# Kernel optimization log

Measured on AMD Instinct MI355X. Metric: run time of the kernel, lower is better.

## Reference

```python
import jax, jax.numpy as jnp
from jax import lax
import numpy as np

K = 3       # kernel_size
STRIDE = 1
PAD = 1
DIL = 1


def setup_inputs() -> dict:
    key = jax.random.key(0)
    k1, k2, k3, k4 = jax.random.split(key, 4)
    B, C, H, W, Co = 8, 128, 64, 64, 128
    x = jax.random.normal(k1, (B, C, H, W), jnp.float32)
    # offset conv: deformable_groups * 2 * K * K = 18 output channels
    w_off = jax.random.normal(k2, (2 * K * K, C, K, K), jnp.float32) * 0.01
    b_off = jax.random.normal(k3, (2 * K * K,), jnp.float32) * 0.01
    w_dcn = jax.random.normal(k4, (Co, C, K, K), jnp.float32) * (1.0 / np.sqrt(C * K * K))
    return {"x": x, "w_off": w_off, "b_off": b_off, "w_dcn": w_dcn}


def _deform_conv(x, w_off, b_off, w_dcn):
    B, C, H, W = x.shape
    Ho = (H + 2 * PAD - DIL * (K - 1) - 1) // STRIDE + 1
    Wo = (W + 2 * PAD - DIL * (K - 1) - 1) // STRIDE + 1
    KK = K * K

    # --- offset branch: standard conv2d ---
    offset = lax.conv_general_dilated(
        x, w_off, window_strides=(STRIDE, STRIDE),
        padding=[(PAD, PAD), (PAD, PAD)], rhs_dilation=(DIL, DIL),
        dimension_numbers=("NCHW", "OIHW", "NCHW"))
    offset = offset + b_off[None, :, None, None]          # [B, 2*KK, Ho, Wo]
    off = offset.reshape(B, KK, 2, Ho, Wo)
    dy, dx = off[:, :, 0], off[:, :, 1]                   # [B, KK, Ho, Wo]

    # --- sampling coordinates: p0 + p_k + offset ---
    ky, kx = jnp.meshgrid(jnp.arange(K), jnp.arange(K), indexing="ij")
    ky = (ky.reshape(-1) * DIL).astype(x.dtype)           # [KK]
    kx = (kx.reshape(-1) * DIL).astype(x.dtype)
    base_y = (jnp.arange(Ho) * STRIDE - PAD).astype(x.dtype)[None, :, None] + ky[:, None, None]
    base_x = (jnp.arange(Wo) * STRIDE - PAD).astype(x.dtype)[None, None, :] + kx[:, None, None]
    y = base_y[None] + dy                                 # [B, KK, Ho, Wo]
    xc = base_x[None] + dx

    y0 = jnp.floor(y)
    x0 = jnp.floor(xc)
    wy = y - y0                                           # bilinear weights
    wx = xc - x0
    y0i = y0.astype(jnp.int32)
    x0i = x0.astype(jnp.int32)

    def sample_one(xb, y0i, x0i, wy, wx):
        # xb: [C, H, W]; index tensors: [KK, Ho, Wo]
        xf = xb.reshape(C, H * W)

        def corner(iy, ix):
            valid = (iy >= 0) & (iy < H) & (ix >= 0) & (ix < W)   # zero padding
            idx = jnp.clip(iy, 0, H - 1) * W + jnp.clip(ix, 0, W - 1)
            v = jnp.take(xf, idx.reshape(-1), axis=1).reshape(C, KK, Ho, Wo)
            return v * valid[None].astype(xb.dtype)

        v00 = corner(y0i, x0i)
        v01 = corner(y0i, x0i + 1)
        v10 = corner(y0i + 1, x0i)
        v11 = corner(y0i + 1, x0i + 1)
        return (v00 * (1 - wy) * (1 - wx) + v01 * (1 - wy) * wx
                + v10 * wy * (1 - wx) + v11 * wy * wx)      # [C, KK, Ho, Wo]

    sampled = jax.vmap(sample_one)(x, y0i, x0i, wy, wx)      # [B, C, KK, Ho, Wo]

    # --- deformable conv accumulation (groups=1, no bias) ---
    w = w_dcn.reshape(w_dcn.shape[0], C, KK)
    return jnp.einsum("bckhw,ock->bohw", sampled, w)


def reference(x, w_off, b_off, w_dcn):
    return _deform_conv(x, w_off, b_off, w_dcn)
```

## Files before the change

### kernel.cpp

```cpp
#include <hip/hip_runtime.h>

typedef float f32x4 __attribute__((ext_vector_type(4)));
typedef int   i32x4 __attribute__((ext_vector_type(4)));
typedef unsigned u32x4 __attribute__((ext_vector_type(4)));
typedef short b16x8 __attribute__((ext_vector_type(8)));

__device__ __forceinline__ short f2b(float v) {
  union { float f; unsigned u; } x; x.f = v;
  unsigned r = x.u + 0x7FFFu + ((x.u >> 16) & 1u);
  return (short)(r >> 16);
}
__device__ __forceinline__ float b2f(short s) {
  union { unsigned u; float f; } x; x.u = ((unsigned)(unsigned short)s) << 16;
  return x.f;
}

#define WT_ELEMS   (9 * 128 * 128)
#define WOFF_ELEMS (9 * 32 * 128)
#define XT_BYTES   (8u * 4096u * 128u * 2u)

#define WIN_OFF   0
#define SS0_OFF   23040
#define SS1_OFF   27136
#define COFS_OFF  31232
#define WTA_OFF   35840
#define ARENA_SZ  40448

__global__ __launch_bounds__(256) void prep_w(
    const float* __restrict__ w_off, const float* __restrict__ w_dcn,
    short* __restrict__ wT, short* __restrict__ wOffT)
{
  int t = blockIdx.x * 256 + threadIdx.x;
  int stride = gridDim.x * 256;
  for (int i = t; i < WT_ELEMS; i += stride) {
    int j    = i & 7;
    int lane = (i >> 3) & 63;
    int kk   = (i >> 9) & 3;
    int og   = (i >> 11) & 7;
    int k    = i >> 14;
    int o = og * 16 + (lane & 15);
    int c = kk * 32 + (lane >> 4) * 8 + j;
    wT[i] = f2b(w_dcn[o * 1152 + c * 9 + k]);
  }
  for (int i = t; i < WOFF_ELEMS; i += stride) {
    int j    = i & 7;
    int lane = (i >> 3) & 63;
    int kk   = (i >> 9) & 3;
    int fo   = (i >> 11) & 1;
    int k    = i >> 12;
    int o = fo * 16 + (lane & 15);
    int c = kk * 32 + (lane >> 4) * 8 + j;
    wOffT[i] = (o < 18) ? f2b(w_off[o * 1152 + c * 9 + k]) : (short)0;
  }
}

__global__ __launch_bounds__(256) void transp(
    const float* __restrict__ xg, short* __restrict__ xt)
{
  __shared__ float tile[32][65];
  const int bid = blockIdx.x;
  const int b = bid >> 6, y = bid & 63;
  const int t = threadIdx.x;
  const float* src = xg + ((size_t)b << 19) + y * 64;
  short*       dst = xt + ((size_t)b << 19) + (size_t)y * 8192;

  for (int ct = 0; ct < 4; ++ct) {
    __syncthreads();
    int c_l = t >> 3, w0 = (t & 7) * 8;
    const float* p = src + (size_t)(ct * 32 + c_l) * 4096 + w0;
    f32x4 a0 = *(const f32x4*)p;
    f32x4 a1 = *(const f32x4*)(p + 4);
    #pragma unroll
    for (int i = 0; i < 4; ++i) { tile[c_l][w0 + i] = a0[i]; tile[c_l][w0 + 4 + i] = a1[i]; }
    __syncthreads();
    int w = t >> 2, j0 = (t & 3) * 8;
    b16x8 pk;
    #pragma unroll
    for (int j = 0; j < 8; ++j) pk[j] = f2b(tile[j0 + j][w]);
    *(b16x8*)(dst + w * 128 + ct * 32 + j0) = pk;
  }
}

__device__ __forceinline__ void lerp_half(char* sbuf, const char* win, const short* xb,
                                          int h, const unsigned* cofsT, const f32x4* wtA,
                                          int k, int px_s, int cg) {
  u32x4 co = *(const u32x4*)&cofsT[(k * 32 + px_s) * 4];
  f32x4 wv = wtA[k * 32 + px_s];
  b16x8 g[4];
  #pragma unroll
  for (int c = 0; c < 4; ++c) {
    unsigned ofs = co[c];
    if (ofs & 0x80000000u) {
      const short* gp = xb + (size_t)(ofs & 0x7fffffffu) * 128 + h * 64 + cg * 8;
      g[c] = *(const b16x8*)gp;
    } else {
      unsigned key = ((ofs >> 7) & 7) << 4;
      g[c] = *(const b16x8*)(win + ofs + ((cg * 16) ^ key));
    }
  }
  b16x8 pk;
  #pragma unroll
  for (int j = 0; j < 8; ++j) {
    float v = wv[0] * b2f(g[0][j]) + wv[1] * b2f(g[1][j]) +
              wv[2] * b2f(g[2][j]) + wv[3] * b2f(g[3][j]);
    pk[j] = f2b(v);
  }
  *(b16x8*)(sbuf + px_s * 128 + ((cg * 16) ^ ((px_s & 7) << 4))) = pk;
}

__device__ __forceinline__ void load_wfrag_half(b16x8 (&w)[4], const short* wT,
                                                int k, int h, int wv_, int lane) {
  const int og0 = wv_ * 2;
  #pragma unroll
  for (int kkl = 0; kkl < 2; ++kkl) {
    w[kkl]     = *(const b16x8*)(wT + ((((k * 8 + og0)     * 4) + 2 * h + kkl) << 9) + lane * 8);
    w[2 + kkl] = *(const b16x8*)(wT + ((((k * 8 + og0 + 1) * 4) + 2 * h + kkl) << 9) + lane * 8);
  }
}

__device__ __forceinline__ void mfma_half(const char* sbuf, const b16x8 (&w)[4],
                                          int l15, int l4,
                                          f32x4& a00, f32x4& a01, f32x4& a10, f32x4& a11) {
  #pragma unroll
  for (int kkl = 0; kkl < 2; ++kkl) {
    int cl2 = kkl * 64 + l4 * 16;
    b16x8 b0 = *(const b16x8*)(sbuf + l15 * 128        + (cl2 ^ ((l15 & 7) << 4)));
    b16x8 b1 = *(const b16x8*)(sbuf + (16 + l15) * 128 + (cl2 ^ ((l15 & 7) << 4)));
    a00 = __builtin_amdgcn_mfma_f32_16x16x32_bf16(w[kkl],     b0, a00, 0, 0, 0);
    a01 = __builtin_amdgcn_mfma_f32_16x16x32_bf16(w[kkl],     b1, a01, 0, 0, 0);
    a10 = __builtin_amdgcn_mfma_f32_16x16x32_bf16(w[2 + kkl], b0, a10, 0, 0, 0);
    a11 = __builtin_amdgcn_mfma_f32_16x16x32_bf16(w[2 + kkl], b1, a11, 0, 0, 0);
  }
}

__global__ __launch_bounds__(256, 4) void dcn_mfma(
    const short* __restrict__ xt, const float* __restrict__ b_off,
    const short* __restrict__ wT, const short* __restrict__ wOffT,
    float* __restrict__ out)
{
  __shared__ __align__(16) char arena[ARENA_SZ];

  char*     sW    = arena + WIN_OFF;
  char*     win   = arena + WIN_OFF;
  char*     sS0   = arena + SS0_OFF;
  char*     sS1   = arena + SS1_OFF;
  float*    offT  = (float*)(arena + SS0_OFF);
  unsigned* cofsT = (unsigned*)(arena + COFS_OFF);
  f32x4*    wtA   = (f32x4*)(arena + WTA_OFF);

  const int tid  = threadIdx.x;
  const int lane = tid & 63;
  const int wv_  = tid >> 6;
  const int bid  = blockIdx.x;
  const int swz  = (bid & 7) * 128 + (bid >> 3);
  const int b    = swz >> 7;
  const int ho   = (swz >> 1) & 63;
  const int wo0  = (swz & 1) * 32;

  const int px_s = tid >> 3;
  const int cg   = tid & 7;
  const int l15  = lane & 15;
  const int l4   = lane >> 4;

  const short* xb = xt + ((size_t)b << 19);

  #pragma unroll 1
  for (int i = 0; i < 7; ++i) {
    int s = tid + i * 256;
    if (s < 1632) {
      int p = s >> 4, cc = s & 15;
      int py = p / 34, pxw = p - py * 34;
      int y = ho - 1 + py, xw = wo0 + pxw - 1;
      bool v = ((unsigned)y < 64u) && ((unsigned)xw < 64u);
      b16x8 q = {0,0,0,0,0,0,0,0};
      if (v) q = *(const b16x8*)(xb + ((size_t)(y * 64 + xw) << 7) + cc * 8);
      *(b16x8*)(sW + p * 256 + ((cc * 16) ^ ((p & 7) << 4))) = q;
    }
  }
  __syncthreads();

  f32x4 accP = {0.f, 0.f, 0.f, 0.f};
  const int fo = wv_ >> 1, fp = wv_ & 1;
  {
    const int bpx = fp * 16 + l15;
    #pragma unroll 1
    for (int k = 0; k < 9; ++k) {
      int ky = k / 3, kx = k - ky * 3;
      int p  = ky * 34 + bpx + kx;
      const short* wkf = wOffT + (((k * 2 + fo) * 4) << 9);
      #pragma unroll
      for (int kk = 0; kk < 4; ++kk) {
        int cf = kk * 32 + l4 * 8;
        b16x8 a  = *(const b16x8*)(wkf + (kk << 9) + lane * 8);
        b16x8 bb = *(const b16x8*)(sW + p * 256 + ((cf * 2) ^ ((p & 7) << 4)));
        accP = __builtin_amdgcn_mfma_f32_16x16x32_bf16(a, bb, accP, 0, 0, 0);
      }
    }
  }
  __syncthreads();
  {
    int px = fp * 16 + l15;
    int ob = fo * 16 + l4 * 4;
    #pragma unroll
    for (int r = 0; r < 4; ++r)
      offT[(ob + r) * 32 + px] = accP[r];
  }
  __syncthreads();

  #pragma unroll 1
  for (int i = 0; i < 2; ++i) {
    int item = tid + i * 256;
    if (item < 288) {
      int k = item >> 5, px = item & 31;
      int ky = k / 3, kx = k - ky * 3;
      float dy = offT[(2 * k) * 32 + px]     + b_off[2 * k];
      float dx = offT[(2 * k + 1) * 32 + px] + b_off[2 * k + 1];
      float yy = (float)(ho - 1 + ky) + dy;
      float xx = (float)(wo0 + px - 1 + kx) + dx;
      float y0f = floorf(yy), x0f = floorf(xx);
      float wy = yy - y0f, wx = xx - x0f;
      int y0 = (int)y0f, x0 = (int)x0f;
      int y1 = y0 + 1, x1 = x0 + 1;
      int cy0 = min(max(y0, 0), 63), cx0 = min(max(x0, 0), 63);
      int cy1 = min(max(y1, 0), 63), cx1 = min(max(x1, 0), 63);
      float vy0 = ((unsigned)y0 < 64u) ? 1.f : 0.f;
      float vy1 = ((unsigned)y1 < 64u) ? 1.f : 0.f;
      float vx0 = ((unsigned)x0 < 64u) ? 1.f : 0.f;
      float vx1 = ((unsigned)x1 < 64u) ? 1.f : 0.f;
      f32x4 wvv;
      wvv[0] = (1.f - wy) * (1.f - wx) * vy0 * vx0;
      wvv[1] = (1.f - wy) * wx         * vy0 * vx1;
      wvv[2] = wy         * (1.f - wx) * vy1 * vx0;
      wvv[3] = wy         * wx         * vy1 * vx1;
      int cys[4] = {cy0, cy0, cy1, cy1};
      int cxs[4] = {cx0, cx1, cx0, cx1};
      u32x4 enc;
      #pragma unroll
      for (int c = 0; c < 4; ++c) {
        int wr = cys[c] - (ho - 2);
        int wc = cxs[c] - (wo0 - 2);
        bool inw = ((unsigned)wr < 5u) && ((unsigned)wc < 36u);
        enc[c] = inw ? (unsigned)((wr * 36 + wc) * 128)
                     : (0x80000000u | (unsigned)(cys[c] * 64 + cxs[c]));
      }
      *(u32x4*)&cofsT[item * 4] = enc;
      wtA[item] = wvv;
    }
  }
  __syncthreads();

  f32x4 acc00 = {0,0,0,0}, acc01 = {0,0,0,0}, acc10 = {0,0,0,0}, acc11 = {0,0,0,0};
  b16x8 wreg[4], wnext[4];
  load_wfrag_half(wreg, wT, 0, 0, wv_, lane);

  #pragma unroll 1
  for (int h = 0; h < 2; ++h) {
    #pragma unroll 1
    for (int i = 0; i < 6; ++i) {
      int s = tid + i * 256;
      if (s < 1440) {
        int seg = s & 7, pos = s >> 3;
        int r = pos / 36, cc = pos - r * 36;
        int y = ho - 2 + r, x = wo0 - 2 + cc;
        bool v = ((unsigned)y < 64u) && ((unsigned)x < 64u);
        b16x8 q = {0,0,0,0,0,0,0,0};
        if (v) q = *(const b16x8*)(xb + ((size_t)(y * 64 + x) << 7) + h * 64 + seg * 8);
        *(b16x8*)(win + pos * 128 + ((seg * 16) ^ ((pos & 7) << 4))) = q;
      }
    }
    __syncthreads();

    #pragma unroll 1
    for (int k = 0; k < 9; ++k) {
      char* sb = ((h * 9 + k) & 1) ? sS1 : sS0;
      lerp_half(sb, win, xb, h, cofsT, wtA, k, px_s, cg);
      if (k < 8)            load_wfrag_half(wnext, wT, k + 1, h, wv_, lane);
      else if (h == 0)      load_wfrag_half(wnext, wT, 0, 1, wv_, lane);
      __syncthreads();
      mfma_half(sb, wreg, l15, l4, acc00, acc01, acc10, acc11);
      #pragma unroll
      for (int i = 0; i < 4; ++i) wreg[i] = wnext[i];
    }
  }

  {
    size_t base = ((size_t)b * 128) * 4096 + (size_t)ho * 64 + wo0;
    int o0 = wv_ * 32 + l4 * 4;
    #pragma unroll
    for (int r = 0; r < 4; ++r) {
      out[base + (size_t)(o0 + r) * 4096 + l15]           = acc00[r];
      out[base + (size_t)(o0 + r) * 4096 + 16 + l15]      = acc01[r];
      out[base + (size_t)(o0 + 16 + r) * 4096 + l15]      = acc10[r];
      out[base + (size_t)(o0 + 16 + r) * 4096 + 16 + l15] = acc11[r];
    }
  }
}

extern "C" void kernel_launch(void* const* d_in, const int* in_sizes, int n_in,
                              void* d_out, int out_size, void* d_ws, size_t ws_size,
                              hipStream_t stream) {
  const float* x     = (const float*)d_in[0];
  const float* w_off = (const float*)d_in[1];
  const float* b_off = (const float*)d_in[2];
  const float* w_dcn = (const float*)d_in[3];
  float* out = (float*)d_out;

  short* xt    = (short*)d_ws;
  short* wT    = (short*)((char*)d_ws + XT_BYTES);
  short* wOffT = (short*)((char*)d_ws + XT_BYTES + WT_ELEMS * 2);

  hipLaunchKernelGGL(prep_w,   dim3(64),   dim3(256), 0, stream, w_off, w_dcn, wT, wOffT);
  hipLaunchKernelGGL(transp,   dim3(512),  dim3(256), 0, stream, x, xt);
  hipLaunchKernelGGL(dcn_mfma, dim3(1024), dim3(256), 0, stream, xt, b_off, wT, wOffT, out);
}
```

Before: 52.08 us.

## Build MFMA B-fragments in registers directly from bilinear sampling

```diff
diff --git a/kernel.cpp b/kernel.cpp
--- a/kernel.cpp
+++ b/kernel.cpp
@@ -20,11 +20,10 @@
 #define XT_BYTES   (8u * 4096u * 128u * 2u)
 
 #define WIN_OFF   0
-#define SS0_OFF   23040
-#define SS1_OFF   27136
-#define COFS_OFF  31232
-#define WTA_OFF   35840
-#define ARENA_SZ  40448
+#define COFS_OFF  23040
+#define WTA_OFF   27648
+#define OFFT_OFF  32256
+#define ARENA_SZ  36352
 
 __global__ __launch_bounds__(256) void prep_w(
     const float* __restrict__ w_off, const float* __restrict__ w_dcn,
@@ -81,56 +80,28 @@
   }
 }
 
-__device__ __forceinline__ void lerp_half(char* sbuf, const char* win, const short* xb,
-                                          int h, const unsigned* cofsT, const f32x4* wtA,
-                                          int k, int px_s, int cg) {
-  u32x4 co = *(const u32x4*)&cofsT[(k * 32 + px_s) * 4];
-  f32x4 wv = wtA[k * 32 + px_s];
+__device__ __forceinline__ b16x8 lerp_frag(const char* win, const short* xb, int h,
+                                           u32x4 co, f32x4 wv, int ccol) {
   b16x8 g[4];
   #pragma unroll
   for (int c = 0; c < 4; ++c) {
     unsigned ofs = co[c];
     if (ofs & 0x80000000u) {
-      const short* gp = xb + (size_t)(ofs & 0x7fffffffu) * 128 + h * 64 + cg * 8;
+      const short* gp = xb + (size_t)(ofs & 0x7fffffffu) * 128 + h * 64 + (ccol >> 1);
       g[c] = *(const b16x8*)gp;
     } else {
       unsigned key = ((ofs >> 7) & 7) << 4;
-      g[c] = *(const b16x8*)(win + ofs + ((cg * 16) ^ key));
-    }
-  }
-  b16x8 pk;
+      g[c] = *(const b16x8*)(win + ofs + (ccol ^ key));
+    }
+  }
+  b16x8 sfrag;
   #pragma unroll
   for (int j = 0; j < 8; ++j) {
     float v = wv[0] * b2f(g[0][j]) + wv[1] * b2f(g[1][j]) +
               wv[2] * b2f(g[2][j]) + wv[3] * b2f(g[3][j]);
-    pk[j] = f2b(v);
-  }
-  *(b16x8*)(sbuf + px_s * 128 + ((cg * 16) ^ ((px_s & 7) << 4))) = pk;
-}
-
-__device__ __forceinline__ void load_wfrag_half(b16x8 (&w)[4], const short* wT,
-                                                int k, int h, int wv_, int lane) {
-  const int og0 = wv_ * 2;
-  #pragma unroll
-  for (int kkl = 0; kkl < 2; ++kkl) {
-    w[kkl]     = *(const b16x8*)(wT + ((((k * 8 + og0)     * 4) + 2 * h + kkl) << 9) + lane * 8);
-    w[2 + kkl] = *(const b16x8*)(wT + ((((k * 8 + og0 + 1) * 4) + 2 * h + kkl) << 9) + lane * 8);
-  }
-}
-
-__device__ __forceinline__ void mfma_half(const char* sbuf, const b16x8 (&w)[4],
-                                          int l15, int l4,
-                                          f32x4& a00, f32x4& a01, f32x4& a10, f32x4& a11) {
-  #pragma unroll
-  for (int kkl = 0; kkl < 2; ++kkl) {
-    int cl2 = kkl * 64 + l4 * 16;
-    b16x8 b0 = *(const b16x8*)(sbuf + l15 * 128        + (cl2 ^ ((l15 & 7) << 4)));
-    b16x8 b1 = *(const b16x8*)(sbuf + (16 + l15) * 128 + (cl2 ^ ((l15 & 7) << 4)));
-    a00 = __builtin_amdgcn_mfma_f32_16x16x32_bf16(w[kkl],     b0, a00, 0, 0, 0);
-    a01 = __builtin_amdgcn_mfma_f32_16x16x32_bf16(w[kkl],     b1, a01, 0, 0, 0);
-    a10 = __builtin_amdgcn_mfma_f32_16x16x32_bf16(w[2 + kkl], b0, a10, 0, 0, 0);
-    a11 = __builtin_amdgcn_mfma_f32_16x16x32_bf16(w[2 + kkl], b1, a11, 0, 0, 0);
-  }
+    sfrag[j] = f2b(v);
+  }
+  return sfrag;
 }
 
 __global__ __launch_bounds__(256, 4) void dcn_mfma(
@@ -142,11 +113,9 @@
 
   char*     sW    = arena + WIN_OFF;
   char*     win   = arena + WIN_OFF;
-  char*     sS0   = arena + SS0_OFF;
-  char*     sS1   = arena + SS1_OFF;
-  float*    offT  = (float*)(arena + SS0_OFF);
   unsigned* cofsT = (unsigned*)(arena + COFS_OFF);
   f32x4*    wtA   = (f32x4*)(arena + WTA_OFF);
+  float*    offT  = (float*)(arena + OFFT_OFF);
 
   const int tid  = threadIdx.x;
   const int lane = tid & 63;
@@ -157,8 +126,6 @@
   const int ho   = (swz >> 1) & 63;
   const int wo0  = (swz & 1) * 32;
 
-  const int px_s = tid >> 3;
-  const int cg   = tid & 7;
   const int l15  = lane & 15;
   const int l4   = lane >> 4;
 
@@ -197,7 +164,6 @@
       }
     }
   }
-  __syncthreads();
   {
     int px = fp * 16 + l15;
     int ob = fo * 16 + l4 * 4;
@@ -249,12 +215,16 @@
   }
   __syncthreads();
 
-  f32x4 acc00 = {0,0,0,0}, acc01 = {0,0,0,0}, acc10 = {0,0,0,0}, acc11 = {0,0,0,0};
-  b16x8 wreg[4], wnext[4];
-  load_wfrag_half(wreg, wT, 0, 0, wv_, lane);
+  const int pxg   = wv_ & 1;
+  const int ohalf = wv_ >> 1;
+  const int mypx  = pxg * 16 + l15;
+  const int ccol0 = l4 * 16;
+
+  f32x4 acc0 = {0,0,0,0}, acc1 = {0,0,0,0}, acc2 = {0,0,0,0}, acc3 = {0,0,0,0};
 
   #pragma unroll 1
   for (int h = 0; h < 2; ++h) {
+    if (h) __syncthreads();
     #pragma unroll 1
     for (int i = 0; i < 6; ++i) {
       int s = tid + i * 256;
@@ -272,26 +242,33 @@
 
     #pragma unroll 1
     for (int k = 0; k < 9; ++k) {
-      char* sb = ((h * 9 + k) & 1) ? sS1 : sS0;
-      lerp_half(sb, win, xb, h, cofsT, wtA, k, px_s, cg);
-      if (k < 8)            load_wfrag_half(wnext, wT, k + 1, h, wv_, lane);
-      else if (h == 0)      load_wfrag_half(wnext, wT, 0, 1, wv_, lane);
-      __syncthreads();
-      mfma_half(sb, wreg, l15, l4, acc00, acc01, acc10, acc11);
+      u32x4 co  = *(const u32x4*)&cofsT[(k * 32 + mypx) * 4];
+      f32x4 wvv = wtA[k * 32 + mypx];
       #pragma unroll
-      for (int i = 0; i < 4; ++i) wreg[i] = wnext[i];
+      for (int kkl = 0; kkl < 2; ++kkl) {
+        b16x8 sfrag = lerp_frag(win, xb, h, co, wvv, kkl * 64 + ccol0);
+        const short* wk = wT + (((k * 8 + ohalf * 4) * 4 + 2 * h + kkl) << 9) + lane * 8;
+        b16x8 w0 = *(const b16x8*)(wk);
+        b16x8 w1 = *(const b16x8*)(wk + (4 << 9));
+        b16x8 w2 = *(const b16x8*)(wk + (8 << 9));
+        b16x8 w3 = *(const b16x8*)(wk + (12 << 9));
+        acc0 = __builtin_amdgcn_mfma_f32_16x16x32_bf16(w0, sfrag, acc0, 0, 0, 0);
+        acc1 = __builtin_amdgcn_mfma_f32_16x16x32_bf16(w1, sfrag, acc1, 0, 0, 0);
+        acc2 = __builtin_amdgcn_mfma_f32_16x16x32_bf16(w2, sfrag, acc2, 0, 0, 0);
+        acc3 = __builtin_amdgcn_mfma_f32_16x16x32_bf16(w3, sfrag, acc3, 0, 0, 0);
+      }
     }
   }
 
   {
-    size_t base = ((size_t)b * 128) * 4096 + (size_t)ho * 64 + wo0;
-    int o0 = wv_ * 32 + l4 * 4;
+    size_t base = ((size_t)b * 128) * 4096 + (size_t)ho * 64 + wo0 + pxg * 16;
+    int o0 = ohalf * 64 + l4 * 4;
     #pragma unroll
     for (int r = 0; r < 4; ++r) {
-      out[base + (size_t)(o0 + r) * 4096 + l15]           = acc00[r];
-      out[base + (size_t)(o0 + r) * 4096 + 16 + l15]      = acc01[r];
-      out[base + (size_t)(o0 + 16 + r) * 4096 + l15]      = acc10[r];
-      out[base + (size_t)(o0 + 16 + r) * 4096 + 16 + l15] = acc11[r];
+      out[base + (size_t)(o0 + r) * 4096 + l15]      = acc0[r];
+      out[base + (size_t)(o0 + 16 + r) * 4096 + l15] = acc1[r];
+      out[base + (size_t)(o0 + 32 + r) * 4096 + l15] = acc2[r];
+      out[base + (size_t)(o0 + 48 + r) * 4096 + l15] = acc3[r];
     }
   }
 }
```

After: 62.53 us. +20.1%, slower.
